# Kernel tuning notes

Hardware: AMD Instinct MI355X
Metric: run time of the kernel (lower is better)

The kernel has to match this reference:

```python
import jax, jax.numpy as jnp
import numpy as np

HIDDEN = 1024
HEADS = 16
HEAD_DIM = HIDDEN // HEADS
EPS = 1e-5


def setup_inputs() -> dict:
    key = jax.random.key(0)
    ks = jax.random.split(key, 9)
    B, S, H = 2, 2048, HIDDEN
    scale = 1.0 / np.sqrt(H)
    inp = {
        "hidden_states": jax.random.normal(ks[0], (B, S, H), dtype=jnp.float32),
        "Wq": jax.random.normal(ks[1], (H, H), dtype=jnp.float32) * scale,
        "bq": jnp.zeros((H,), jnp.float32),
        "Wk": jax.random.normal(ks[2], (H, H), dtype=jnp.float32) * scale,
        "bk": jnp.zeros((H,), jnp.float32),
        "Wv": jax.random.normal(ks[3], (H, H), dtype=jnp.float32) * scale,
        "bv": jnp.zeros((H,), jnp.float32),
        "Wo": jax.random.normal(ks[4], (H, H), dtype=jnp.float32) * scale,
        "bo": jnp.zeros((H,), jnp.float32),
        "gamma": jnp.ones((H,), jnp.float32),
        "beta": jnp.zeros((H,), jnp.float32),
    }
    return inp


def reference(hidden_states, Wq, bq, Wk, bk, Wv, bv, Wo, bo, gamma, beta):
    B, S, H = hidden_states.shape
    residual = hidden_states

    def shape(x):  # [B,S,H] -> [B,heads,S,head_dim]
        return x.reshape(B, S, HEADS, HEAD_DIM).transpose(0, 2, 1, 3)

    q = shape(hidden_states @ Wq + bq)
    k = shape(hidden_states @ Wk + bk)
    v = shape(hidden_states @ Wv + bv)

    scores = jnp.einsum("bhqd,bhkd->bhqk", q, k) / jnp.sqrt(
        jnp.asarray(HEAD_DIM, hidden_states.dtype))
    probs = jax.nn.softmax(scores, axis=-1)
    context = jnp.einsum("bhqk,bhkd->bhqd", probs, v)
    context = context.transpose(0, 2, 1, 3).reshape(B, S, H)

    output = context @ Wo + bo
    x = output + residual
    mu = jnp.mean(x, axis=-1, keepdims=True)
    var = jnp.mean(jnp.square(x - mu), axis=-1, keepdims=True)
    return (x - mu) * jax.lax.rsqrt(var + EPS) * gamma + beta
```

## Files before the change

kernel.cpp:

```cpp
#include <hip/hip_runtime.h>
#include <hip/hip_bf16.h>
#include <math.h>

#define HIDDEN 1024
#define HEADS 16
#define HEAD_DIM 64
#define EPS 1e-5f

typedef __attribute__((ext_vector_type(8))) short bf16x8;
typedef __attribute__((ext_vector_type(4))) float f32x4;

#if defined(__has_builtin)
#if __has_builtin(__builtin_amdgcn_exp2f)
#define EXP2(x) __builtin_amdgcn_exp2f(x)
#endif
#endif
#ifndef EXP2
#define EXP2(x) exp2f(x)
#endif

#define QSCALE 0.18033688011112042f

__device__ __forceinline__ short f2bf(float f) {
    union { float f; unsigned u; } v; v.f = f;
    unsigned r = v.u + 0x7fffu + ((v.u >> 16) & 1u);
    return (short)(r >> 16);
}

__device__ __forceinline__ void gl_lds16(const void* g, void* l) {
    __builtin_amdgcn_global_load_lds(
        (const __attribute__((address_space(1))) void*)g,
        (__attribute__((address_space(3))) void*)l, 16, 0, 0);
}

__global__ __launch_bounds__(256) void cast_bf16_kernel(
    const float* __restrict__ in, short* __restrict__ out, int n)
{
    int i = (blockIdx.x * 256 + threadIdx.x) * 4;
    if (i >= n) return;
    float4 v = *(const float4*)(in + i);
    short o[4] = { f2bf(v.x), f2bf(v.y), f2bf(v.z), f2bf(v.w) };
    *(uint2*)(out + i) = *(uint2*)o;
}

__global__ __launch_bounds__(256) void wtrans_kernel(
    const float* __restrict__ Wq, const float* __restrict__ Wk,
    const float* __restrict__ Wv, const float* __restrict__ Wo,
    short* __restrict__ Wt3, short* __restrict__ Wot)
{
    const int wsel = blockIdx.z;
    const float* W = (wsel == 0) ? Wq : (wsel == 1) ? Wk : (wsel == 2) ? Wv : Wo;
    short* dst = (wsel < 3) ? (Wt3 + (size_t)wsel * 1024 * 1024) : Wot;
    const float scale = (wsel == 0) ? QSCALE : 1.0f;

    __shared__ short tile[32][33];
    int n0 = blockIdx.x * 32;
    int k0 = blockIdx.y * 32;
    int tx = threadIdx.x & 31;
    int ty = threadIdx.x >> 5;
    #pragma unroll
    for (int i = 0; i < 32; i += 8)
        tile[ty + i][tx] = f2bf(W[(size_t)(k0 + ty + i) * 1024 + n0 + tx] * scale);
    __syncthreads();
    #pragma unroll
    for (int i = 0; i < 32; i += 8)
        dst[(size_t)(n0 + ty + i) * 1024 + k0 + tx] = tile[tx][ty + i];
}

__global__ __launch_bounds__(256) void concat_bias_kernel(
    const float* __restrict__ bq, const float* __restrict__ bk,
    const float* __restrict__ bv, float* __restrict__ b3)
{
    int i = blockIdx.x * 256 + threadIdx.x;
    if (i >= 3072) return;
    float v = (i < 1024) ? bq[i] * QSCALE
            : (i < 2048) ? bk[i - 1024] : bv[i - 2048];
    b3[i] = v;
}

__global__ __launch_bounds__(256) void gemm_bt_mfma(
    const short* __restrict__ A, const short* __restrict__ Bt,
    const float* __restrict__ bias,
    void* __restrict__ C0, int ldc0,
    void* __restrict__ C1, int split_col, int ldc1,
    const float* __restrict__ resid,
    int M, int N, int K, int out_bf16)
{
    __shared__ short As[128 * 32];
    __shared__ short Bs[128 * 32];
    const int tid = threadIdx.x;
    const int wave = tid >> 6, lane = tid & 63;
    const int ln16 = lane & 15, quad = lane >> 4;
    const int wm = (wave >> 1) * 64, wn = (wave & 1) * 64;
    const int brow = blockIdx.y * 128, bcol = blockIdx.x * 128;

    const int sr  = lane >> 2;
    const int scb = lane & 3;

    f32x4 acc[4][4];
    #pragma unroll
    for (int mt = 0; mt < 4; ++mt)
        #pragma unroll
        for (int nt = 0; nt < 4; ++nt) acc[mt][nt] = (f32x4){0.f, 0.f, 0.f, 0.f};

    for (int k0 = 0; k0 < K; k0 += 32) {
        __syncthreads();
        #pragma unroll
        for (int i = 0; i < 2; ++i) {
            int rb = i * 64 + wave * 16;
            int r  = rb + sr;
            int csrc = (scb ^ ((r >> 1) & 3)) * 8;
            gl_lds16(A  + (size_t)(brow + r) * K + k0 + csrc, &As[rb * 32]);
            gl_lds16(Bt + (size_t)(bcol + r) * K + k0 + csrc, &Bs[rb * 32]);
        }
        __syncthreads();

        bf16x8 af[4], bf[4];
        #pragma unroll
        for (int mt = 0; mt < 4; ++mt) {
            int r = wm + mt * 16 + ln16;
            af[mt] = *(const bf16x8*)&As[r * 32 + ((quad ^ ((r >> 1) & 3)) * 8)];
        }
        #pragma unroll
        for (int nt = 0; nt < 4; ++nt) {
            int r = wn + nt * 16 + ln16;
            bf[nt] = *(const bf16x8*)&Bs[r * 32 + ((quad ^ ((r >> 1) & 3)) * 8)];
        }
        #pragma unroll
        for (int mt = 0; mt < 4; ++mt)
            #pragma unroll
            for (int nt = 0; nt < 4; ++nt)
                acc[mt][nt] = __builtin_amdgcn_mfma_f32_16x16x32_bf16(
                    af[mt], bf[nt], acc[mt][nt], 0, 0, 0);
    }

    void* Cp = C0; int ld = ldc0; int coff = 0;
    if (bcol >= split_col) { Cp = C1; ld = ldc1; coff = split_col; }

    #pragma unroll
    for (int mt = 0; mt < 4; ++mt) {
        #pragma unroll
        for (int r = 0; r < 4; ++r) {
            int row = brow + wm + mt * 16 + quad * 4 + r;
            #pragma unroll
            for (int nt = 0; nt < 4; ++nt) {
                int col = bcol + wn + nt * 16 + ln16;
                float v = acc[mt][nt][r] + bias[col];
                if (resid) v += resid[(size_t)row * N + col];
                if (out_bf16) ((short*)Cp)[(size_t)row * ld + (col - coff)] = f2bf(v);
                else          ((float*)Cp)[(size_t)row * ld + (col - coff)] = v;
            }
        }
    }
}

__global__ __launch_bounds__(256) void vtranspose_kernel(
    const short* __restrict__ Vb, short* __restrict__ VT)
{
    __shared__ short t[64][72];
    const int c0 = blockIdx.x * 64;
    const int r0 = blockIdx.y * 64;
    const int tid = threadIdx.x;
    #pragma unroll
    for (int i = 0; i < 2; ++i) {
        int idx = tid + i * 256;
        int r = idx >> 3, cc = (idx & 7) * 8;
        *(uint4*)&t[r][cc] = *(const uint4*)(Vb + (size_t)(r0 + r) * 1024 + c0 + cc);
    }
    __syncthreads();
    #pragma unroll
    for (int i = 0; i < 2; ++i) {
        int idx = tid + i * 256;
        int c = idx >> 3, rr = (idx & 7) * 8;
        short tmp[8];
        #pragma unroll
        for (int j = 0; j < 8; ++j) tmp[j] = t[rr + j][c];
        *(uint4*)(VT + (size_t)(c0 + c) * 4096 + r0 + rr) = *(uint4*)tmp;
    }
}

__global__ __launch_bounds__(256, 3) void attn_mfma_kernel(
    const short* __restrict__ QKb, const short* __restrict__ VT,
    short* __restrict__ Ctx)
{
    const int S = 2048;
    const int h = blockIdx.x, qt = blockIdx.y, b = blockIdx.z;
    const int tid = threadIdx.x;
    const int wave = tid >> 6, lane = tid & 63;
    const int ln16 = lane & 15, quad = lane >> 4;

    __shared__ alignas(16) char smem[20480];
    char* Pw = smem + wave * 4096;

    bf16x8 qf[4][2];
    #pragma unroll
    for (int qg = 0; qg < 4; ++qg)
        #pragma unroll
        for (int kb = 0; kb < 2; ++kb)
            qf[qg][kb] = *(const bf16x8*)(QKb +
                (size_t)(b * S + qt * 64 + qg * 16 + ln16) * 2048 +
                h * 64 + kb * 32 + quad * 8);

    bf16x8 ones;
    #pragma unroll
    for (int j = 0; j < 8; ++j) ones[j] = (short)0x3F80;

    f32x4 of[4][4], lacc[4];
    #pragma unroll
    for (int qg = 0; qg < 4; ++qg) {
        lacc[qg] = (f32x4){0.f, 0.f, 0.f, 0.f};
        #pragma unroll
        for (int nt = 0; nt < 4; ++nt) of[qg][nt] = (f32x4){0.f, 0.f, 0.f, 0.f};
    }

    const short* Kbase = QKb + (size_t)b * S * 2048 + 1024 + h * 64;
    const short* Vbase = VT + (size_t)(h * 64) * 4096 + (size_t)b * S;

    #pragma unroll 1
    for (int it = 0; it < 16; ++it) {
        const int t0 = wave * 512 + it * 32;

        #pragma unroll
        for (int kblk = 0; kblk < 2; ++kblk) {
            const short* krow = Kbase + (size_t)(t0 + kblk * 16 + ln16) * 2048;
            bf16x8 kf0 = *(const bf16x8*)(krow + quad * 8);
            bf16x8 kf1 = *(const bf16x8*)(krow + 32 + quad * 8);
            #pragma unroll
            for (int qg = 0; qg < 4; ++qg) {
                f32x4 a = (f32x4){0.f, 0.f, 0.f, 0.f};
                a = __builtin_amdgcn_mfma_f32_16x16x32_bf16(kf0, qf[qg][0], a, 0, 0, 0);
                a = __builtin_amdgcn_mfma_f32_16x16x32_bf16(kf1, qf[qg][1], a, 0, 0, 0);
                float p0 = EXP2(a[0]), p1 = EXP2(a[1]);
                float p2 = EXP2(a[2]), p3 = EXP2(a[3]);
                union { __hip_bfloat162 h2; unsigned u; } c01, c23;
                c01.h2 = __float22bfloat162_rn(make_float2(p0, p1));
                c23.h2 = __float22bfloat162_rn(make_float2(p2, p3));
                uint2 w; w.x = c01.u; w.y = c23.u;
                int row = qg * 16 + ln16;
                int blk = (kblk * 2 + (quad >> 1)) ^ (row & 3);
                *(uint2*)(Pw + row * 64 + blk * 16 + (quad & 1) * 8) = w;
            }
        }

        bf16x8 pf[4];
        #pragma unroll
        for (int qg = 0; qg < 4; ++qg) {
            int row = qg * 16 + ln16;
            int blk = quad ^ (row & 3);
            pf[qg] = *(const bf16x8*)(Pw + row * 64 + blk * 16);
            lacc[qg] = __builtin_amdgcn_mfma_f32_16x16x32_bf16(pf[qg], ones, lacc[qg], 0, 0, 0);
        }
        #pragma unroll
        for (int nt = 0; nt < 4; ++nt) {
            bf16x8 vf = *(const bf16x8*)(Vbase + (size_t)(nt * 16 + ln16) * 4096 + t0 + quad * 8);
            #pragma unroll
            for (int qg = 0; qg < 4; ++qg)
                of[qg][nt] = __builtin_amdgcn_mfma_f32_16x16x32_bf16(pf[qg], vf, of[qg][nt], 0, 0, 0);
        }
    }

    __syncthreads();

    float* Rw = (float*)(smem + wave * 4864);
    float* Lb = (float*)(smem + 4 * 4864);

    if (ln16 == 0) {
        #pragma unroll
        for (int qg = 0; qg < 4; ++qg)
            #pragma unroll
            for (int r = 0; r < 4; ++r)
                Lb[wave * 64 + qg * 16 + quad * 4 + r] = lacc[qg][r];
    }

    const int rq  = tid >> 2;
    const int rd0 = (tid & 3) * 4;
    float inv = 0.f;

    #pragma unroll
    for (int nt = 0; nt < 4; ++nt) {
        #pragma unroll
        for (int qg = 0; qg < 4; ++qg)
            #pragma unroll
            for (int r = 0; r < 4; ++r)
                Rw[(qg * 16 + quad * 4 + r) * 19 + ln16] = of[qg][nt][r];
        __syncthreads();
        if (nt == 0) {
            float l = Lb[rq] + Lb[64 + rq] + Lb[128 + rq] + Lb[192 + rq];
            inv = 1.f / l;
        }
        short o4[4];
        #pragma unroll
        for (int j = 0; j < 4; ++j) {
            int d = rd0 + j;
            float s = 0.f;
            #pragma unroll
            for (int w = 0; w < 4; ++w)
                s += ((const float*)(smem + w * 4864))[rq * 19 + d];
            o4[j] = f2bf(s * inv);
        }
        *(uint2*)(Ctx + (size_t)(b * S + qt * 64 + rq) * 1024 + h * 64 + nt * 16 + rd0) =
            *(uint2*)o4;
        __syncthreads();
    }
}

__global__ __launch_bounds__(256) void resln_kernel(
    const float* __restrict__ xin, const float* __restrict__ gamma,
    const float* __restrict__ beta, float* __restrict__ out)
{
    const int row = blockIdx.x;
    const int tid = threadIdx.x;
    const int wid = tid >> 6, lane = tid & 63;
    __shared__ float red[8];

    float4 x = *(const float4*)(xin + (size_t)row * HIDDEN + tid * 4);
    float s = x.x + x.y + x.z + x.w;
    #pragma unroll
    for (int off = 32; off > 0; off >>= 1) s += __shfl_xor(s, off, 64);
    if (lane == 0) red[wid] = s;
    __syncthreads();
    float mu = (red[0] + red[1] + red[2] + red[3]) * (1.f / HIDDEN);

    float dx = x.x - mu, dy = x.y - mu, dz = x.z - mu, dw = x.w - mu;
    float v = dx * dx + dy * dy + dz * dz + dw * dw;
    #pragma unroll
    for (int off = 32; off > 0; off >>= 1) v += __shfl_xor(v, off, 64);
    if (lane == 0) red[4 + wid] = v;
    __syncthreads();
    float var = (red[4] + red[5] + red[6] + red[7]) * (1.f / HIDDEN);
    float rstd = rsqrtf(var + EPS);

    float4 g = *(const float4*)(gamma + tid * 4);
    float4 bt = *(const float4*)(beta + tid * 4);
    float4 o;
    o.x = dx * rstd * g.x + bt.x;
    o.y = dy * rstd * g.y + bt.y;
    o.z = dz * rstd * g.z + bt.z;
    o.w = dw * rstd * g.w + bt.w;
    *(float4*)(out + (size_t)row * HIDDEN + tid * 4) = o;
}

extern "C" void kernel_launch(void* const* d_in, const int* in_sizes, int n_in,
                              void* d_out, int out_size, void* d_ws, size_t ws_size,
                              hipStream_t stream)
{
    const float* X     = (const float*)d_in[0];
    const float* Wq    = (const float*)d_in[1];
    const float* bq    = (const float*)d_in[2];
    const float* Wk    = (const float*)d_in[3];
    const float* bk    = (const float*)d_in[4];
    const float* Wv    = (const float*)d_in[5];
    const float* bv    = (const float*)d_in[6];
    const float* Wo    = (const float*)d_in[7];
    const float* bo    = (const float*)d_in[8];
    const float* gamma = (const float*)d_in[9];
    const float* beta  = (const float*)d_in[10];
    float* out = (float*)d_out;

    const int B = 2, S = 2048;
    const int M = B * S;
    const size_t mat = (size_t)M * HIDDEN;

    char* ws = (char*)d_ws;
    short* Xb  = (short*)(ws);
    short* VT  = (short*)(ws);
    short* Wot = (short*)(ws + (8ull << 20));
    short* Wt3 = (short*)(ws + (10ull << 20));
    float* b3  = (float*)(ws + (16ull << 20));
    short* QKb = (short*)(ws + (17ull << 20));
    float* Pj  = (float*)(ws + (17ull << 20));
    short* Vb  = (short*)(ws + (33ull << 20));
    short* Ctx = (short*)(ws + (33ull << 20));

    dim3 blk(256);

    cast_bf16_kernel<<<dim3((int)(mat / 4 / 256)), blk, 0, stream>>>(X, Xb, (int)mat);
    wtrans_kernel<<<dim3(32, 32, 4), blk, 0, stream>>>(Wq, Wk, Wv, Wo, Wt3, Wot);
    concat_bias_kernel<<<12, blk, 0, stream>>>(bq, bk, bv, b3);

    dim3 qkvgrid(3072 / 128, M / 128);
    gemm_bt_mfma<<<qkvgrid, blk, 0, stream>>>(Xb, Wt3, b3,
                                              QKb, 2048, Vb, 2048, 1024,
                                              nullptr, M, 3072, HIDDEN, 1);

    vtranspose_kernel<<<dim3(16, 64), blk, 0, stream>>>(Vb, VT);

    dim3 agrid(HEADS, S / 64, B);
    attn_mfma_kernel<<<agrid, blk, 0, stream>>>(QKb, VT, Ctx);

    dim3 ogrid(HIDDEN / 128, M / 128);
    gemm_bt_mfma<<<ogrid, blk, 0, stream>>>(Ctx, Wot, bo,
                                            Pj, 1024, nullptr, 1 << 30, 0,
                                            X, M, HIDDEN, HIDDEN, 0);

    resln_kernel<<<M, blk, 0, stream>>>(Pj, gamma, beta, out);
}
```

Baseline: 261.3 us.

## Double-buffer K/V tiles in LDS via async global-to-LDS loads

The attention kernel now stages 128-key K and V^T tiles into a double-buffered shared-memory ring with direct global-to-LDS loads, using XOR swizzles. Each wave computes from LDS instead of issuing scattered global loads per MFMA step, and the next tile is prefetched while the current one is computed. The P-tile swizzle is also changed to reduce bank conflicts. In exchange, LDS use rises to 80KB, which drops the occupancy hint from 3 to 2 blocks, and two block-wide barriers are added per iteration.

```diff
diff --git a/kernel.cpp b/kernel.cpp
--- a/kernel.cpp
+++ b/kernel.cpp
@@ -179,7 +179,7 @@
     }
 }
 
-__global__ __launch_bounds__(256, 3) void attn_mfma_kernel(
+__global__ __launch_bounds__(256, 2) void attn_mfma_kernel(
     const short* __restrict__ QKb, const short* __restrict__ VT,
     short* __restrict__ Ctx)
 {
@@ -189,8 +189,8 @@
     const int wave = tid >> 6, lane = tid & 63;
     const int ln16 = lane & 15, quad = lane >> 4;
 
-    __shared__ alignas(16) char smem[20480];
-    char* Pw = smem + wave * 4096;
+    __shared__ alignas(16) char smem[81920];
+    char* Pw = smem + 65536 + wave * 4096;
 
     bf16x8 qf[4][2];
     #pragma unroll
@@ -213,18 +213,49 @@
         for (int nt = 0; nt < 4; ++nt) of[qg][nt] = (f32x4){0.f, 0.f, 0.f, 0.f};
     }
 
-    const short* Kbase = QKb + (size_t)b * S * 2048 + 1024 + h * 64;
-    const short* Vbase = VT + (size_t)(h * 64) * 4096 + (size_t)b * S;
-
-    #pragma unroll 1
-    for (int it = 0; it < 16; ++it) {
-        const int t0 = wave * 512 + it * 32;
+    auto stage = [&](int p, int kt) {
+        short* ksb = (short*)(smem + p * 16384);
+        short* vsb = (short*)(smem + 32768 + p * 16384);
+        const int kr  = lane >> 3;
+        const int kb8 = lane & 7;
+        const int vr  = lane >> 4;
+        const int vb16 = lane & 15;
+        #pragma unroll
+        for (int i = 0; i < 4; ++i) {
+            int r = wave * 32 + i * 8 + kr;
+            int ksrc = (kb8 ^ (r & 7)) * 8;
+            gl_lds16(QKb + (size_t)(b * S + kt * 128 + r) * 2048 + 1024 + h * 64 + ksrc,
+                     ksb + (wave * 32 + i * 8) * 64);
+            int d = wave * 16 + i * 4 + vr;
+            int vsrc = (vb16 ^ (d & 15)) * 8;
+            gl_lds16(VT + (size_t)(h * 64 + d) * 4096 + b * S + kt * 128 + vsrc,
+                     vsb + (wave * 16 + i * 4) * 128);
+        }
+    };
+
+    stage(0, 0);
+
+    for (int kt = 0; kt < 16; ++kt) {
+        const int p = kt & 1;
+
+        if (kt + 1 < 16) {
+            stage(p ^ 1, kt + 1);
+            asm volatile("s_waitcnt vmcnt(8)" ::: "memory");
+        } else {
+            asm volatile("s_waitcnt vmcnt(0)" ::: "memory");
+        }
+        __builtin_amdgcn_s_barrier();
+        __builtin_amdgcn_sched_barrier(0);
+
+        const short* ks = (const short*)(smem + p * 16384);
+        const short* vs = (const short*)(smem + 32768 + p * 16384);
+        const int t0w = wave * 32;
 
         #pragma unroll
         for (int kblk = 0; kblk < 2; ++kblk) {
-            const short* krow = Kbase + (size_t)(t0 + kblk * 16 + ln16) * 2048;
-            bf16x8 kf0 = *(const bf16x8*)(krow + quad * 8);
-            bf16x8 kf1 = *(const bf16x8*)(krow + 32 + quad * 8);
+            int rloc = t0w + kblk * 16 + ln16;
+            bf16x8 kf0 = *(const bf16x8*)&ks[rloc * 64 + ((quad ^ (rloc & 7)) * 8)];
+            bf16x8 kf1 = *(const bf16x8*)&ks[rloc * 64 + (((4 + quad) ^ (rloc & 7)) * 8)];
             #pragma unroll
             for (int qg = 0; qg < 4; ++qg) {
                 f32x4 a = (f32x4){0.f, 0.f, 0.f, 0.f};
@@ -236,27 +267,32 @@
                 c01.h2 = __float22bfloat162_rn(make_float2(p0, p1));
                 c23.h2 = __float22bfloat162_rn(make_float2(p2, p3));
                 uint2 w; w.x = c01.u; w.y = c23.u;
-                int row = qg * 16 + ln16;
-                int blk = (kblk * 2 + (quad >> 1)) ^ (row & 3);
-                *(uint2*)(Pw + row * 64 + blk * 16 + (quad & 1) * 8) = w;
+                int qrow = qg * 16 + ln16;
+                int key = (qrow >> 1) & 3;
+                int bblk = (kblk * 2 + (quad >> 1)) ^ key;
+                *(uint2*)(Pw + qrow * 64 + bblk * 16 + (quad & 1) * 8) = w;
             }
         }
 
         bf16x8 pf[4];
         #pragma unroll
         for (int qg = 0; qg < 4; ++qg) {
-            int row = qg * 16 + ln16;
-            int blk = quad ^ (row & 3);
-            pf[qg] = *(const bf16x8*)(Pw + row * 64 + blk * 16);
+            int qrow = qg * 16 + ln16;
+            int key = (qrow >> 1) & 3;
+            pf[qg] = *(const bf16x8*)(Pw + qrow * 64 + ((quad ^ key) * 16));
             lacc[qg] = __builtin_amdgcn_mfma_f32_16x16x32_bf16(pf[qg], ones, lacc[qg], 0, 0, 0);
         }
         #pragma unroll
         for (int nt = 0; nt < 4; ++nt) {
-            bf16x8 vf = *(const bf16x8*)(Vbase + (size_t)(nt * 16 + ln16) * 4096 + t0 + quad * 8);
+            int d = nt * 16 + ln16;
+            bf16x8 vf = *(const bf16x8*)&vs[d * 128 + (((wave * 4 + quad) ^ (d & 15)) * 8)];
             #pragma unroll
             for (int qg = 0; qg < 4; ++qg)
                 of[qg][nt] = __builtin_amdgcn_mfma_f32_16x16x32_bf16(pf[qg], vf, of[qg][nt], 0, 0, 0);
         }
+
+        __builtin_amdgcn_sched_barrier(0);
+        __builtin_amdgcn_s_barrier();
     }
 
     __syncthreads();
```

After: 250.6 us. -4.1%, faster.
